# Optimization experiments

Hardware: AMD Instinct MI355X
Metric: run time of the kernel (lower is better)

## Reference

```python
import jax, jax.numpy as jnp
import numpy as np

COMMITMENT_COST = 0.25
ENTROPY_LOSS_RATIO = 0.1
ENTROPY_TEMPERATURE = 0.01


def setup_inputs() -> dict:
    key = jax.random.key(0)
    k1, k2 = jax.random.split(key)
    x = jax.random.normal(k1, (64, 32, 32, 256), dtype=jnp.float32)
    # variance_scaling(fan_in, uniform) init for the codebook parameter
    codebook_size, emb_dim = 1024, 256
    limit = jnp.sqrt(3.0 / emb_dim)
    codebook = jax.random.uniform(k2, (codebook_size, emb_dim), jnp.float32, -limit, limit)
    return {"x": x, "codebook": codebook}


def _squared_euclidean_distance(a, b):
    # a: (n, d), b: (m, d) -> (n, m)
    a2 = jnp.sum(a * a, axis=1, keepdims=True)          # (n, 1)
    b2 = jnp.sum(b * b, axis=1)[None, :]                # (1, m)
    ab = jnp.matmul(a, b.T)                             # (n, m)
    return a2 - 2.0 * ab + b2


def _entropy_loss(affinity, temperature):
    # affinity: (..., K); loss_type='softmax'
    flat = affinity.reshape(-1, affinity.shape[-1]) / temperature
    probs = jax.nn.softmax(flat, axis=-1)
    log_probs = jax.nn.log_softmax(flat + 1e-05, axis=-1)
    target_probs = probs
    avg_probs = jnp.mean(target_probs, axis=0)
    avg_entropy = -jnp.sum(avg_probs * jnp.log(avg_probs + 1e-05))
    sample_entropy = -jnp.mean(jnp.sum(target_probs * log_probs, axis=-1))
    return sample_entropy - avg_entropy


def reference(x, codebook):
    sg = jax.lax.stop_gradient
    emb_dim = x.shape[-1]
    codebook_size = codebook.shape[0]
    flat_x = x.reshape(-1, emb_dim)                              # (N, d)
    distances = _squared_euclidean_distance(flat_x, codebook)    # (N, K)
    distances = distances.reshape(x.shape[:-1] + (codebook_size,))
    encoding_indices = jnp.argmin(distances, axis=-1)            # (B,H,W) int
    # quantize: onehot @ codebook == gather of codebook rows
    quantized = jnp.take(codebook, encoding_indices, axis=0)     # (B,H,W,d)

    e_latent_loss = jnp.mean((sg(quantized) - x) ** 2) * COMMITMENT_COST
    q_latent_loss = jnp.mean((quantized - sg(x)) ** 2)
    entropy_loss = _entropy_loss(-distances, ENTROPY_TEMPERATURE) * ENTROPY_LOSS_RATIO
    loss = (e_latent_loss + q_latent_loss + entropy_loss).astype(jnp.float32)

    # straight-through estimator
    quantized = x + sg(quantized - x)
    return quantized, loss, encoding_indices
```

## Files before the change

### kernel.cpp

```cpp
#include <hip/hip_runtime.h>
#include <math.h>

#define NROWS 65536
#define DIM   256
#define KCB   1024
#define TM    64
#define NBLK  (NROWS / TM)
#define QOFF  (NROWS * DIM)
#define IDXOFF (QOFF + 1)

#define WS_DMIN 0
#define WS_PLP  1
#define WS_AVGP 4
#define WS_C2   (WS_AVGP + 8 * 1024)
#define WS_CBF  (WS_C2 + 1024)

#define DELTA 0.05f
#define XPITCH 260

typedef __attribute__((ext_vector_type(8))) __bf16 bf16x8;
typedef __attribute__((ext_vector_type(4))) float  f32x4;
typedef __attribute__((ext_vector_type(8))) unsigned short u16x8;

#define EP_REDD 0
#define EP_REDK 512
#define EP_RT1  1024
#define EP_RT2  1536
#define EP_GMIN 2048
#define EP_CNT  2112
#define EP_CAND 2176
#define EP_CEX  3200
#define EP_R1F  4224
#define EP_SP   4288
#define EP_KFIN 4352
#define EP_DFIN 4416
#define EP_AVGP 4480
#define EP_SIZE 5504

__device__ __forceinline__ unsigned short f2bf(float f) {
    unsigned u = __float_as_uint(f);
    u += 0x7fffu + ((u >> 16) & 1u);
    return (unsigned short)(u >> 16);
}

__device__ __forceinline__ bf16x8 cvt8(const float* src) {
    float4 v0 = *(const float4*)src, v1 = *(const float4*)(src + 4);
    u16x8 o;
    o[0] = f2bf(v0.x); o[1] = f2bf(v0.y); o[2] = f2bf(v0.z); o[3] = f2bf(v0.w);
    o[4] = f2bf(v1.x); o[5] = f2bf(v1.y); o[6] = f2bf(v1.z); o[7] = f2bf(v1.w);
    return __builtin_bit_cast(bf16x8, o);
}

__device__ __forceinline__ void gload_lds16(const void* g, void* l) {
    __builtin_amdgcn_global_load_lds(
        (const __attribute__((address_space(1))) unsigned int*)g,
        (__attribute__((address_space(3))) unsigned int*)l, 16, 0, 0);
}

__global__ __launch_bounds__(256) void prep_kernel(const float* __restrict__ cb,
                                                   float* __restrict__ ws) {
    int gid = blockIdx.x * 256 + threadIdx.x;
    if (gid < 4) ws[gid] = 0.f;
    if (gid < 8192) ws[WS_AVGP + gid] = 0.f;

    int k  = gid >> 5;
    int s  = gid & 31;
    int kc = s >> 2;
    int qq = s & 3;

    if (gid < 1024) {
        const float4* row = (const float4*)(cb + (size_t)gid * DIM);
        float ssum = 0.f;
#pragma unroll 8
        for (int i = 0; i < DIM / 4; ++i) {
            float4 v = row[i];
            ssum += v.x * v.x + v.y * v.y + v.z * v.z + v.w * v.w;
        }
        ws[WS_C2 + gid] = ssum;
    }

    unsigned short* cbf = (unsigned short*)(ws + WS_CBF);
    const float* src = cb + (size_t)k * DIM + (kc << 5) + (qq << 3);
    float4 v0 = *(const float4*)src, v1 = *(const float4*)(src + 4);
    u16x8 o;
    o[0] = f2bf(v0.x); o[1] = f2bf(v0.y); o[2] = f2bf(v0.z); o[3] = f2bf(v0.w);
    o[4] = f2bf(v1.x); o[5] = f2bf(v1.y); o[6] = f2bf(v1.z); o[7] = f2bf(v1.w);
    *(u16x8*)(cbf + ((((size_t)(kc << 10) + k) << 2) + qq) * 8) = o;
}

__global__ __launch_bounds__(1024, 4) void vq_main(const float* __restrict__ x,
                                                   const float* __restrict__ cb,
                                                   float* __restrict__ ws,
                                                   float* __restrict__ out) {
    __shared__ float epi[EP_SIZE];
    __shared__ float xs[64 * XPITCH];
    __shared__ u16x8 ldsB[2][2048];

    const int tid  = threadIdx.x;
    const int w    = tid >> 6;
    const int lane = tid & 63;
    const int m    = lane & 15;
    const int q    = lane >> 4;
    const int wc   = w & 7;
    const int rh   = w >> 3;
    const int R0   = blockIdx.x * TM;

    const char* gB = (const char*)(ws + WS_CBF);
    const int fragoff = (wc << 8) + (m << 2) + q;

    bf16x8 ah[2];

    float4 t0 = *((const float4*)(x + (size_t)(R0 + (w << 2) + 0) * DIM) + lane);
    float4 t1 = *((const float4*)(x + (size_t)(R0 + (w << 2) + 1) * DIM) + lane);
    float4 t2 = *((const float4*)(x + (size_t)(R0 + (w << 2) + 2) * DIM) + lane);
    float4 t3 = *((const float4*)(x + (size_t)(R0 + (w << 2) + 3) * DIM) + lane);

    {
        const char* g = gB + (size_t)tid * 16;
        char* l = (char*)&ldsB[0][0] + (w << 10);
        gload_lds16(g, l);
        gload_lds16(g + 16384, l + 16384);
    }

    *((float4*)(xs + ((w << 2) + 0) * XPITCH) + lane) = t0;
    *((float4*)(xs + ((w << 2) + 1) * XPITCH) + lane) = t1;
    *((float4*)(xs + ((w << 2) + 2) * XPITCH) + lane) = t2;
    *((float4*)(xs + ((w << 2) + 3) * XPITCH) + lane) = t3;

    f32x4 acc[2][8];
#pragma unroll
    for (int a = 0; a < 2; ++a)
#pragma unroll
        for (int b = 0; b < 8; ++b) acc[a][b] = (f32x4)0.f;

    __syncthreads();

    const int rbase = rh << 5;
    ah[0] = cvt8(xs + (rbase + m) * XPITCH + (q << 3));
    ah[1] = cvt8(xs + (rbase + 16 + m) * XPITCH + (q << 3));

#pragma unroll
    for (int sub = 0; sub < 16; ++sub) {
        const int cur = sub & 1;
        if (sub < 15) {
            const char* g = gB + (size_t)(sub + 1) * 32768 + (size_t)tid * 16;
            char* l = (char*)&ldsB[cur ^ 1][0] + (w << 10);
            gload_lds16(g, l);
            gload_lds16(g + 16384, l + 16384);
        }
        const u16x8* lbc = &ldsB[cur][fragoff];
        u16x8 f0 = lbc[0], f1 = lbc[64], f2 = lbc[128], f3 = lbc[192];
#pragma unroll
        for (int ct = 0; ct < 4; ++ct) {
            u16x8 fr = (ct == 0) ? f0 : (ct == 1) ? f1 : (ct == 2) ? f2 : f3;
            bf16x8 bh = __builtin_bit_cast(bf16x8, fr);
            int cg = ((sub & 1) << 2) + ct;
            acc[0][cg] = __builtin_amdgcn_mfma_f32_16x16x32_bf16(ah[0], bh, acc[0][cg], 0, 0, 0);
            acc[1][cg] = __builtin_amdgcn_mfma_f32_16x16x32_bf16(ah[1], bh, acc[1][cg], 0, 0, 0);
        }
        if ((sub & 1) == 1 && sub < 15) {
            const int nkc = (sub >> 1) + 1;
            ah[0] = cvt8(xs + (rbase + m) * XPITCH + (nkc << 5) + (q << 3));
            ah[1] = cvt8(xs + (rbase + 16 + m) * XPITCH + (nkc << 5) + (q << 3));
        }
        if (sub < 15) __syncthreads();
    }

    if (tid < 64) ((int*)(epi + EP_CNT))[tid] = 0;
    epi[EP_AVGP + tid] = 0.f;

    float c2v[8];
#pragma unroll
    for (int cg = 0; cg < 8; ++cg) {
        int col = ((cg >> 2) << 9) + (wc << 6) + ((cg & 3) << 4) + m;
        c2v[cg] = ws[WS_C2 + col];
    }
#pragma unroll
    for (int rt = 0; rt < 2; ++rt) {
#pragma unroll
        for (int reg = 0; reg < 4; ++reg) {
            int row = rbase + (rt << 4) + (q << 2) + reg;
            float md = 3.0e38f; int mk = 0;
#pragma unroll
            for (int cg = 0; cg < 8; ++cg) {
                float g = c2v[cg] - 2.0f * acc[rt][cg][reg];
                acc[rt][cg][reg] = g;
                int col = ((cg >> 2) << 9) + (wc << 6) + ((cg & 3) << 4) + m;
                if (g < md) { md = g; mk = col; }
            }
#pragma unroll
            for (int off = 1; off <= 8; off <<= 1) {
                float od = __shfl_xor(md, off, 64);
                int   ok = __shfl_xor(mk, off, 64);
                if (od < md || (od == md && ok < mk)) { md = od; mk = ok; }
            }
            if (m == 0) {
                epi[EP_REDD + (wc << 6) + row] = md;
                ((int*)(epi + EP_REDK))[(wc << 6) + row] = mk;
            }
        }
    }
    __syncthreads();

    if (tid < 64) {
        float gm = 3.0e38f;
#pragma unroll
        for (int g = 0; g < 8; ++g) {
            float d = epi[EP_REDD + (g << 6) + tid];
            if (d < gm) gm = d;
        }
        epi[EP_GMIN + tid] = gm;
    }
    __syncthreads();

    {
        int* cnt  = (int*)(epi + EP_CNT);
        int* cand = (int*)(epi + EP_CAND);
#pragma unroll
        for (int rt = 0; rt < 2; ++rt) {
#pragma unroll
            for (int reg = 0; reg < 4; ++reg) {
                int row = rbase + (rt << 4) + (q << 2) + reg;
                float gm = epi[EP_GMIN + row];
                float t1 = 0.f, t2 = 0.f;
#pragma unroll
                for (int cg = 0; cg < 8; ++cg) {
                    float g = acc[rt][cg][reg];
                    if (g < gm + DELTA) {
                        int col = ((cg >> 2) << 9) + (wc << 6) + ((cg & 3) << 4) + m;
                        int pos = atomicAdd(&cnt[row], 1);
                        if (pos < 16) cand[(row << 4) + pos] = col;
                    }
                    float z = -100.0f * (g - gm);
                    float e = __expf(z);
                    acc[rt][cg][reg] = e;
                    t1 += e;
                    t2 += e * z;
                }
#pragma unroll
                for (int off = 1; off <= 8; off <<= 1) {
                    t1 += __shfl_xor(t1, off, 64);
                    t2 += __shfl_xor(t2, off, 64);
                }
                if (m == 0) {
                    epi[EP_RT1 + (wc << 6) + row] = t1;
                    epi[EP_RT2 + (wc << 6) + row] = t2;
                }
            }
        }
    }
    __syncthreads();

    if (tid < 64) {
        float T1 = 0.f, T2 = 0.f;
#pragma unroll
        for (int g = 0; g < 8; ++g) {
            T1 += epi[EP_RT1 + (g << 6) + tid];
            T2 += epi[EP_RT2 + (g << 6) + tid];
        }
        float r1 = 1.0f / T1;
        epi[EP_R1F + tid] = r1;
        epi[EP_SP + tid]  = T2 * r1 - logf(T1);
    }
    __syncthreads();

    float sv[8];
    {
        float r1v[2][4];
#pragma unroll
        for (int rt = 0; rt < 2; ++rt)
#pragma unroll
            for (int reg = 0; reg < 4; ++reg)
                r1v[rt][reg] = epi[EP_R1F + rbase + (rt << 4) + (q << 2) + reg];
#pragma unroll
        for (int cg = 0; cg < 8; ++cg) {
            float s = 0.f;
#pragma unroll
            for (int rt = 0; rt < 2; ++rt)
#pragma unroll
                for (int reg = 0; reg < 4; ++reg)
                    s += acc[rt][cg][reg] * r1v[rt][reg];
            s += __shfl_xor(s, 16, 64);
            s += __shfl_xor(s, 32, 64);
            sv[cg] = s;
        }
        if (rh == 0 && lane < 16) {
#pragma unroll
            for (int cg = 0; cg < 8; ++cg) {
                int col = ((cg >> 2) << 9) + (wc << 6) + ((cg & 3) << 4) + m;
                epi[EP_AVGP + col] += sv[cg];
            }
        }
    }
    {
        int* cnt  = (int*)(epi + EP_CNT);
        int* cand = (int*)(epi + EP_CAND);
        int r = tid >> 4;
        int i = tid & 15;
        int n = cnt[r]; if (n > 16) n = 16;
        if (i < n) {
            int k = cand[(r << 4) + i];
            const float4* ax = (const float4*)(xs + r * XPITCH);
            const float4* bx = (const float4*)(cb + (((size_t)k) << 8));
            float ab = 0.f, x2 = 0.f;
#pragma unroll 8
            for (int d4 = 0; d4 < 64; ++d4) {
                float4 a = ax[d4], b = bx[d4];
                ab = fmaf(a.x, b.x, ab);
                ab = fmaf(a.y, b.y, ab);
                ab = fmaf(a.z, b.z, ab);
                ab = fmaf(a.w, b.w, ab);
                x2 += a.x * a.x + a.y * a.y + a.z * a.z + a.w * a.w;
            }
            float t = 2.0f * ab;
            epi[EP_CEX + (r << 4) + i] = (x2 - t) + ws[WS_C2 + k];
        }
    }
    __syncthreads();

    if (rh == 1 && lane < 16) {
#pragma unroll
        for (int cg = 0; cg < 8; ++cg) {
            int col = ((cg >> 2) << 9) + (wc << 6) + ((cg & 3) << 4) + m;
            epi[EP_AVGP + col] += sv[cg];
        }
    }

    if (tid < 64) {
        int* cnt  = (int*)(epi + EP_CNT);
        int* cand = (int*)(epi + EP_CAND);
        int n = cnt[tid]; if (n > 16) n = 16;
        float bd = epi[EP_CEX + (tid << 4)];
        int   bk = cand[(tid << 4)];
        for (int i = 1; i < n; ++i) {
            float d = epi[EP_CEX + (tid << 4) + i];
            int   k = cand[(tid << 4) + i];
            if (d < bd || (d == bd && k < bk)) { bd = d; bk = k; }
        }
        ((int*)(epi + EP_KFIN))[tid] = bk;
        epi[EP_DFIN + tid] = bd;
        out[IDXOFF + R0 + tid] = (float)bk;
    }
    __syncthreads();

#pragma unroll
    for (int rr = 0; rr < 4; ++rr) {
        int r = (w << 2) + rr;
        int k = ((int*)(epi + EP_KFIN))[r];
        f32x4 v = *((const f32x4*)(cb + (((size_t)k) << 8)) + lane);
        __builtin_nontemporal_store(v, (f32x4*)(out + (((size_t)(R0 + r)) << 8)) + lane);
    }
    atomicAdd(ws + WS_AVGP + ((blockIdx.x & 7) << 10) + tid, epi[EP_AVGP + tid]);
    if (tid < 64) {
        float sp = epi[EP_SP + tid];
        float dd = epi[EP_DFIN + tid];
#pragma unroll
        for (int off = 1; off <= 32; off <<= 1) {
            sp += __shfl_xor(sp, off, 64);
            dd += __shfl_xor(dd, off, 64);
        }
        if (tid == 0) {
            atomicAdd(ws + WS_PLP, sp);
            atomicAdd(ws + WS_DMIN, dd);
        }
    }
}

__global__ __launch_bounds__(256) void vq_finalize(const float* __restrict__ ws,
                                                   float* __restrict__ out) {
    __shared__ float red[4];
    int tid = threadIdx.x;
    float part = 0.f;
    for (int k = tid; k < 1024; k += 256) {
        float s = 0.f;
#pragma unroll
        for (int r = 0; r < 8; ++r) s += ws[WS_AVGP + (r << 10) + k];
        float ap = s * (1.0f / 65536.0f);
        part += ap * logf(ap + 1e-5f);
    }
#pragma unroll
    for (int off = 32; off; off >>= 1) part += __shfl_xor(part, off, 64);
    if ((tid & 63) == 0) red[tid >> 6] = part;
    __syncthreads();
    if (tid == 0) {
        float sum_aplog      = red[0] + red[1] + red[2] + red[3];
        float avg_entropy    = -sum_aplog;
        float sample_entropy = -ws[WS_PLP] * (1.0f / 65536.0f);
        float entropy_loss   = (sample_entropy - avg_entropy) * 0.1f;
        float eq = 1.25f * ws[WS_DMIN] * (1.0f / ((float)NROWS * (float)DIM));
        out[QOFF] = eq + entropy_loss;
    }
}

extern "C" void kernel_launch(void* const* d_in, const int* in_sizes, int n_in,
                              void* d_out, int out_size, void* d_ws, size_t ws_size,
                              hipStream_t stream) {
    const float* x  = (const float*)d_in[0];
    const float* cb = (const float*)d_in[1];
    float* out = (float*)d_out;
    float* ws  = (float*)d_ws;

    prep_kernel<<<128, 256, 0, stream>>>(cb, ws);
    vq_main<<<NBLK, 1024, 0, stream>>>(x, cb, ws, out);
    vq_finalize<<<1, 256, 0, stream>>>(ws, out);
}
```

Before: 248.8 us.

## Fuse finalize into main kernel via last-block counter and relayout bf16 codebook

Removes the separate finalize kernel launch: each block increments a global counter after its atomics, and the last block reduces the average-probability histogram and writes the loss. The prep kernel now writes the bf16 codebook in a fragment-contiguous order so each lane's fragment offset is simply its lane index, which makes the per-wave loads contiguous. This saves one kernel launch and its gap. In exchange it adds a threadfence, an extra barrier and a counter atomic to every block, and the final reduction runs serially in a single block.

```diff
diff --git a/kernel.cpp b/kernel.cpp
--- a/kernel.cpp
+++ b/kernel.cpp
@@ -11,6 +11,7 @@
 
 #define WS_DMIN 0
 #define WS_PLP  1
+#define WS_CTR  2
 #define WS_AVGP 4
 #define WS_C2   (WS_AVGP + 8 * 1024)
 #define WS_CBF  (WS_C2 + 1024)
@@ -63,11 +64,6 @@
     if (gid < 4) ws[gid] = 0.f;
     if (gid < 8192) ws[WS_AVGP + gid] = 0.f;
 
-    int k  = gid >> 5;
-    int s  = gid & 31;
-    int kc = s >> 2;
-    int qq = s & 3;
-
     if (gid < 1024) {
         const float4* row = (const float4*)(cb + (size_t)gid * DIM);
         float ssum = 0.f;
@@ -79,13 +75,23 @@
         ws[WS_C2 + gid] = ssum;
     }
 
+    int sub = gid >> 11;
+    int r   = gid & 2047;
+    int wc  = r >> 8;
+    int ct  = (r >> 6) & 3;
+    int qq  = (r >> 4) & 3;
+    int m   = r & 15;
+    int kc  = sub >> 1;
+    int h   = sub & 1;
+    int k   = (h << 9) + (wc << 6) + (ct << 4) + m;
+
     unsigned short* cbf = (unsigned short*)(ws + WS_CBF);
     const float* src = cb + (size_t)k * DIM + (kc << 5) + (qq << 3);
     float4 v0 = *(const float4*)src, v1 = *(const float4*)(src + 4);
     u16x8 o;
     o[0] = f2bf(v0.x); o[1] = f2bf(v0.y); o[2] = f2bf(v0.z); o[3] = f2bf(v0.w);
     o[4] = f2bf(v1.x); o[5] = f2bf(v1.y); o[6] = f2bf(v1.z); o[7] = f2bf(v1.w);
-    *(u16x8*)(cbf + ((((size_t)(kc << 10) + k) << 2) + qq) * 8) = o;
+    *(u16x8*)(cbf + (size_t)gid * 8) = o;
 }
 
 __global__ __launch_bounds__(1024, 4) void vq_main(const float* __restrict__ x,
@@ -106,7 +112,7 @@
     const int R0   = blockIdx.x * TM;
 
     const char* gB = (const char*)(ws + WS_CBF);
-    const int fragoff = (wc << 8) + (m << 2) + q;
+    const int fragoff = (wc << 8) + lane;
 
     bf16x8 ah[2];
 
@@ -364,31 +370,33 @@
             atomicAdd(ws + WS_DMIN, dd);
         }
     }
-}
-
-__global__ __launch_bounds__(256) void vq_finalize(const float* __restrict__ ws,
-                                                   float* __restrict__ out) {
-    __shared__ float red[4];
-    int tid = threadIdx.x;
-    float part = 0.f;
-    for (int k = tid; k < 1024; k += 256) {
+
+    __threadfence();
+    __syncthreads();
+    if (tid == 0) {
+        unsigned old = atomicAdd((unsigned int*)(ws + WS_CTR), 1u);
+        ((int*)xs)[0] = (old == (unsigned)(NBLK - 1)) ? 1 : 0;
+    }
+    __syncthreads();
+    if (((int*)xs)[0]) {
         float s = 0.f;
 #pragma unroll
-        for (int r = 0; r < 8; ++r) s += ws[WS_AVGP + (r << 10) + k];
+        for (int r = 0; r < 8; ++r) s += atomicAdd(ws + WS_AVGP + (r << 10) + tid, 0.f);
         float ap = s * (1.0f / 65536.0f);
-        part += ap * logf(ap + 1e-5f);
-    }
-#pragma unroll
-    for (int off = 32; off; off >>= 1) part += __shfl_xor(part, off, 64);
-    if ((tid & 63) == 0) red[tid >> 6] = part;
-    __syncthreads();
-    if (tid == 0) {
-        float sum_aplog      = red[0] + red[1] + red[2] + red[3];
-        float avg_entropy    = -sum_aplog;
-        float sample_entropy = -ws[WS_PLP] * (1.0f / 65536.0f);
-        float entropy_loss   = (sample_entropy - avg_entropy) * 0.1f;
-        float eq = 1.25f * ws[WS_DMIN] * (1.0f / ((float)NROWS * (float)DIM));
-        out[QOFF] = eq + entropy_loss;
+        float part = ap * logf(ap + 1e-5f);
+#pragma unroll
+        for (int off = 1; off <= 32; off <<= 1) part += __shfl_xor(part, off, 64);
+        if (lane == 0) epi[w] = part;
+        __syncthreads();
+        if (tid == 0) {
+            float sum_aplog = 0.f;
+            for (int i = 0; i < 16; ++i) sum_aplog += epi[i];
+            float avg_entropy    = -sum_aplog;
+            float sample_entropy = -atomicAdd(ws + WS_PLP, 0.f) * (1.0f / 65536.0f);
+            float entropy_loss   = (sample_entropy - avg_entropy) * 0.1f;
+            float eq = 1.25f * atomicAdd(ws + WS_DMIN, 0.f) * (1.0f / ((float)NROWS * (float)DIM));
+            out[QOFF] = eq + entropy_loss;
+        }
     }
 }
 
@@ -402,5 +410,4 @@
 
     prep_kernel<<<128, 256, 0, stream>>>(cb, ws);
     vq_main<<<NBLK, 1024, 0, stream>>>(x, cb, ws, out);
-    vq_finalize<<<1, 256, 0, stream>>>(ws, out);
-}
+}
```

Measured after the change: 664.7 us. 2.67x slower.
